# Kernel optimization log

Measured on AMD Instinct MI355X. Metric: run time of the kernel, lower is better.

The kernel has to match this reference:

```python
import math
import jax, jax.numpy as jnp
import numpy as np

B, T, C, H = 2, 1024, 1024, 16
D = C // H
BASE_SCALE = 0.03125
ATTN_ALPHA_INIT, MLP_ALPHA_INIT = 0.05, 0.05


def sinusoidal_embeddings(n, d):
    pos = jnp.arange(n, dtype=jnp.float32)[:, None]
    div = jnp.exp(jnp.arange(0, d, 2, dtype=jnp.float32) * (-math.log(10000.0) / d))
    emb = jnp.zeros((n, d), dtype=jnp.float32)
    emb = emb.at[:, 0::2].set(jnp.sin(pos * div))
    emb = emb.at[:, 1::2].set(jnp.cos(pos * div))
    return emb


def apply_rope(pos, q):
    # pos: (T, D); q: (B, H, T, D). Faithful to source: returns only the rotated-scaled component.
    pos = pos[-q.shape[2]:]
    d = q.shape[-1]
    sin, cos = pos[:, : d // 2], pos[:, d // 2 :]
    q_rot = jnp.stack((-q[..., 1::2], q[..., ::2]), axis=-1)  # (B,H,T,D/2,2)
    sc = jnp.stack((cos, sin), axis=-1)  # (T, D/2, 2)
    return (q_rot * sc).reshape(q.shape)


def justnorm(x):
    return x / jnp.linalg.norm(x, axis=-1, keepdims=True)


def setup_inputs() -> dict:
    key = jax.random.key(0)
    ks = jax.random.split(key, 14)
    w = lambda k, shape: jax.random.normal(k, shape, jnp.float32) * 0.02
    return {
        "h": jax.random.normal(ks[0], (B, T, C), jnp.float32),
        "Wq": w(ks[1], (C, C)),
        "Wk": w(ks[2], (C, C)),
        "Wv": w(ks[3], (C, C)),
        "Wo": w(ks[4], (C, C)),
        "Wfc": w(ks[5], (8 * C, C)),
        "Wproj": w(ks[6], (C, 4 * C)),
        "sqk": BASE_SCALE * jnp.ones(C) + w(ks[7], (C,)) * 0.05,
        "suv": jnp.ones(8 * C) + w(ks[8], (8 * C,)) * 0.05,
        "attn_alpha": BASE_SCALE * jnp.ones(C) + w(ks[9], (C,)) * 0.05,
        "mlp_alpha": BASE_SCALE * jnp.ones(C) + w(ks[10], (C,)) * 0.05,
        "thr_c": 1.6 * jnp.ones(H) + w(ks[11], (H,)) * 0.5,
        "stp": 10.0 * jnp.ones(H),
    }


def reference(h, Wq, Wk, Wv, Wo, Wfc, Wproj, sqk, suv, attn_alpha, mlp_alpha, thr_c, stp):
    softmax_scale = math.sqrt(D)  # nGPT uses sqrt(head_dim) since q,k are unit-normalized

    # --- attention branch (no pre-norm in nGPT mode) ---
    q = (h @ Wq.T).reshape(B, T, H, D).transpose(0, 2, 1, 3)  # (B,H,T,D)
    k = (h @ Wk.T).reshape(B, T, H, D).transpose(0, 2, 1, 3)
    v = (h @ Wv.T).reshape(B, T, H, D).transpose(0, 2, 1, 3)

    pos = sinusoidal_embeddings(T, D)
    q = apply_rope(pos, q)
    k = apply_rope(pos, k)

    sqk_s = (sqk * (1.0 / BASE_SCALE)).reshape(1, H, 1, D)
    q = sqk_s * justnorm(q)
    k = sqk_s * justnorm(k)

    scores = jnp.einsum("bhqd,bhkd->bhqk", q, k) * softmax_scale  # (B,H,T,T)
    causal = jnp.tril(jnp.ones((T, T), dtype=bool))
    w = jax.nn.softmax(jnp.where(causal, scores, -1e9), axis=-1)
    # soft score threshold: per-head sigmoid gate on raw scores, then renormalize
    gate = jax.nn.sigmoid(stp[None, :, None, None] * (scores - thr_c[None, :, None, None]))
    w = w * gate
    w = w / jnp.sum(w, axis=-1, keepdims=True)

    y = jnp.einsum("bhqk,bhkd->bhqd", w, v).transpose(0, 2, 1, 3).reshape(B, T, C)
    h_att = y @ Wo.T

    lr = jnp.abs(attn_alpha * (ATTN_ALPHA_INIT / BASE_SCALE))
    A = justnorm(h)
    Bn = justnorm(h_att)
    h = justnorm(A + lr * (Bn - A))

    # --- MLP branch ---
    uv = h @ Wfc.T  # (B,T,8C)
    uv = (suv * math.sqrt(C)) * uv
    u, vv = jnp.split(uv, 2, axis=-1)
    x_mlp = u * (vv * jax.nn.sigmoid(vv))
    h_mlp = x_mlp @ Wproj.T

    lr2 = jnp.abs(mlp_alpha * (MLP_ALPHA_INIT / BASE_SCALE))
    A = justnorm(h)
    Bn = justnorm(h_mlp)
    h = justnorm(A + lr2 * (Bn - A))
    return h
```

## Files before the change

kernel.cpp:

```cpp
#include <hip/hip_runtime.h>
#include <hip/hip_bf16.h>
#include <math.h>

typedef _Float16 f16x8 __attribute__((ext_vector_type(8)));
typedef float f32x4 __attribute__((ext_vector_type(4)));
typedef float f32x2 __attribute__((ext_vector_type(2)));
typedef unsigned short u16;
typedef unsigned int u32;
typedef u16 u16x4 __attribute__((ext_vector_type(4)));
typedef u16 u16x8 __attribute__((ext_vector_type(8)));

#define DEVI static __device__ __forceinline__
#define LDSS 72
#define MB (1u << 20)

DEVI u16 f2h(float f) {
    _Float16 h = (_Float16)f;
    return __builtin_bit_cast(u16, h);
}
DEVI float h2f(u16 u) {
    return (float)__builtin_bit_cast(_Float16, u);
}
DEVI f32x4 mfma16(f16x8 a, f16x8 b, f32x4 c) {
    return __builtin_amdgcn_mfma_f32_16x16x32_f16(a, b, c, 0, 0, 0);
}
DEVI void gload16(const u16* g, u16* l) {
    __builtin_amdgcn_global_load_lds((const __attribute__((address_space(1))) void*)g,
                                     (__attribute__((address_space(3))) void*)l, 16, 0, 0);
}

DEVI void stage128(const u16* __restrict__ g, size_t row0, int ldg, int k0, u16* lds) {
    int t = threadIdx.x;
    const u16* src = g + (row0 + (size_t)(t >> 3)) * (size_t)ldg + k0 + (t & 7) * 8;
    u16* dst = lds + (t >> 6) * 512;
#pragma unroll
    for (int is = 0; is < 4; is++)
        gload16(src + (size_t)is * 32 * ldg, dst + is * 2048);
}

DEVI void gemm128_core(const u16* __restrict__ A, const u16* __restrict__ B,
                       int ldk, int kbeg, int kend, int m0, int n0,
                       u16* As, u16* Bs, f32x4 acc[4][4]) {
    int lane = threadIdx.x & 63, w = threadIdx.x >> 6;
    int wm = (w >> 1) * 64, wn = (w & 1) * 64;
    int lrow = lane & 15, lg = lane >> 4;
    for (int k0 = kbeg; k0 < kend; k0 += 64) {
        __syncthreads();
        stage128(A, m0, ldk, k0, As);
        stage128(B, n0, ldk, k0, Bs);
        __syncthreads();
#pragma unroll
        for (int ks = 0; ks < 2; ks++) {
            f16x8 af[4], bf[4];
#pragma unroll
            for (int i = 0; i < 4; i++) {
                af[i] = *reinterpret_cast<f16x8*>(&As[(wm + i * 16 + lrow) * 64 + ks * 32 + lg * 8]);
                bf[i] = *reinterpret_cast<f16x8*>(&Bs[(wn + i * 16 + lrow) * 64 + ks * 32 + lg * 8]);
            }
#pragma unroll
            for (int i = 0; i < 4; i++)
#pragma unroll
                for (int j = 0; j < 4; j++)
                    acc[i][j] = mfma16(af[i], bf[j], acc[i][j]);
        }
    }
}

__global__ void cvt_kernel(const float* __restrict__ h, const float* __restrict__ Wq,
                           const float* __restrict__ Wk, const float* __restrict__ Wv,
                           const float* __restrict__ Wo, const float* __restrict__ Wfc,
                           const float* __restrict__ Wproj, u16* __restrict__ dst) {
    int bid = blockIdx.x;
    const float* src;
    size_t doff;
    int sb;
    if (bid < 1024)      { src = h;     sb = 0;    doff = 0; }
    else if (bid < 1536) { src = Wq;    sb = 1024; doff = 2097152; }
    else if (bid < 2048) { src = Wk;    sb = 1536; doff = 3145728; }
    else if (bid < 2560) { src = Wv;    sb = 2048; doff = 4194304; }
    else if (bid < 3072) { src = Wo;    sb = 2560; doff = 5242880; }
    else if (bid < 7168) { src = Wfc;   sb = 3072; doff = 10485760; }
    else                 { src = Wproj; sb = 7168; doff = 6291456; }
    size_t idx = (size_t)(bid - sb) * 2048 + threadIdx.x * 8;
    f32x4 a = *reinterpret_cast<const f32x4*>(src + idx);
    f32x4 b = *reinterpret_cast<const f32x4*>(src + idx + 4);
    u16x8 o;
    o[0] = f2h(a[0]); o[1] = f2h(a[1]); o[2] = f2h(a[2]); o[3] = f2h(a[3]);
    o[4] = f2h(b[0]); o[5] = f2h(b[1]); o[6] = f2h(b[2]); o[7] = f2h(b[3]);
    *reinterpret_cast<u16x8*>(dst + doff + idx) = o;
}

__global__ __launch_bounds__(256, 2) void qkv_h_kernel(
    const u16* __restrict__ hb, const u16* __restrict__ Wqh, const u16* __restrict__ Wkh,
    const u16* __restrict__ Wvh, u16* __restrict__ qb, u16* __restrict__ kb, u16* __restrict__ vb) {
    __shared__ u16 As[128 * 64];
    __shared__ u16 Bs[128 * 64];
    int z = blockIdx.z;
    const u16* W = (z == 0) ? Wqh : (z == 1) ? Wkh : Wvh;
    u16* dst = (z == 0) ? qb : (z == 1) ? kb : vb;
    int m0 = blockIdx.y * 128, n0 = blockIdx.x * 128;
    f32x4 acc[4][4];
    f32x4 zf = {0.f, 0.f, 0.f, 0.f};
#pragma unroll
    for (int i = 0; i < 4; i++)
#pragma unroll
        for (int j = 0; j < 4; j++) acc[i][j] = zf;
    gemm128_core(hb, W, 1024, 0, 1024, m0, n0, As, Bs, acc);
    int lane = threadIdx.x & 63, w = threadIdx.x >> 6;
    int wm = (w >> 1) * 64, wn = (w & 1) * 64;
    int lrow = lane & 15, lg = lane >> 4;
#pragma unroll
    for (int i = 0; i < 4; i++)
#pragma unroll
        for (int j = 0; j < 4; j++)
#pragma unroll
            for (int r = 0; r < 4; r++) {
                int m = m0 + wm + i * 16 + lg * 4 + r;
                int n = n0 + wn + j * 16 + lrow;
                dst[(size_t)m * 1024 + n] = f2h(acc[i][j][r]);
            }
}

__global__ __launch_bounds__(256, 2) void gemm_h_kernel(
    const u16* __restrict__ A, const u16* __restrict__ B, u16* __restrict__ out,
    int ldk, int ksplit, int osplit, int N) {
    __shared__ u16 As[128 * 64];
    __shared__ u16 Bs[128 * 64];
    int z = blockIdx.z;
    int m0 = blockIdx.y * 128, n0 = blockIdx.x * 128;
    f32x4 acc[4][4];
    f32x4 zf = {0.f, 0.f, 0.f, 0.f};
#pragma unroll
    for (int i = 0; i < 4; i++)
#pragma unroll
        for (int j = 0; j < 4; j++) acc[i][j] = zf;
    gemm128_core(A, B, ldk, z * ksplit, (z + 1) * ksplit, m0, n0, As, Bs, acc);
    u16* o = out + (size_t)z * osplit;
    int lane = threadIdx.x & 63, w = threadIdx.x >> 6;
    int wm = (w >> 1) * 64, wn = (w & 1) * 64;
    int lrow = lane & 15, lg = lane >> 4;
#pragma unroll
    for (int i = 0; i < 4; i++)
#pragma unroll
        for (int j = 0; j < 4; j++)
#pragma unroll
            for (int r = 0; r < 4; r++) {
                int m = m0 + wm + i * 16 + lg * 4 + r;
                int n = n0 + wn + j * 16 + lrow;
                o[(size_t)m * N + n] = f2h(acc[i][j][r]);
            }
}

__global__ void qkprep_kernel(u16* __restrict__ qb, u16* __restrict__ kb,
                              const float* __restrict__ sqk) {
    u16* buf = blockIdx.z ? kb : qb;
    int pair = blockIdx.x * 4 + (threadIdx.x >> 6);
    int m = pair >> 4, hh = pair & 15;
    int tt = m & 1023;
    int d = threadIdx.x & 63;
    size_t off = (size_t)m * 1024 + hh * 64 + d;
    float x = h2f(buf[off]);
    float xn = __shfl_xor(x, 1);
    int j = (d & 1) ? ((d - 1) >> 1) : (32 + (d >> 1));
    float dv = exp2f(-(float)(j >> 1) * 0.41524101186092029f);
    float ang = (float)tt * dv;
    float e = (j & 1) ? cosf(ang) : sinf(ang);
    float xr = (d & 1) ? (xn * e) : (-xn * e);
    float ss = xr * xr;
#pragma unroll
    for (int o = 1; o < 64; o <<= 1) ss += __shfl_xor(ss, o);
    float sc = rsqrtf(ss) * sqk[hh * 64 + d] * 32.0f;
    buf[off] = f2h(xr * sc);
}

__global__ __launch_bounds__(128) void attn_kernel(
    const u16* __restrict__ qb, const u16* __restrict__ kb, const u16* __restrict__ vb,
    const float* __restrict__ thr_c, const float* __restrict__ stp,
    float* __restrict__ yp, f32x2* __restrict__ mden) {
    const int T = 1024, C = 1024;
    int qt = 31 - (blockIdx.x >> 1);
    int c = blockIdx.x & 1;
    int bh = blockIdx.y;
    int b = bh >> 4, hh = bh & 15;
    int q0 = qt * 32;
    int nkt = (q0 >> 6) + 1;
    __shared__ u16 Vt[64 * LDSS];
    __shared__ u16 Ps[32 * LDSS];
    int t = threadIdx.x;
    int lane = t & 63, w = t >> 6;
    int lrow = lane & 15, lg = lane >> 4, lk = lg * 8;

    const u16* qrowp = qb + (size_t)(b * T + q0 + w * 16 + lrow) * C + hh * 64;
    f16x8 qfr[2];
    qfr[0] = *reinterpret_cast<const f16x8*>(qrowp + lk);
    qfr[1] = *reinterpret_cast<const f16x8*>(qrowp + 32 + lk);

    float thr = thr_c[hh], st = stp[hh];
    float st8 = st * 8.0f, stthr = st * thr;
    float mrun = -1e30f, den = 0.f;
    f32x4 yacc[4];
    f32x4 zf = {0.f, 0.f, 0.f, 0.f};
#pragma unroll
    for (int i = 0; i < 4; i++) yacc[i] = zf;
    int qg = q0 + w * 16 + lrow;

    for (int kt = c; kt < nkt; kt += 2) {
        int kv0 = kt << 6;
        __syncthreads();
        {
            int kvp = t & 31, db = t >> 5;
            const u16* src = vb + (size_t)(b * T + kv0 + 2 * kvp) * C + hh * 64 + db * 16;
#pragma unroll
            for (int dd = 0; dd < 4; dd++) {
                u16x4 a = *reinterpret_cast<const u16x4*>(src + dd * 4);
                u16x4 bb = *reinterpret_cast<const u16x4*>(src + C + dd * 4);
#pragma unroll
                for (int e = 0; e < 4; e++) {
                    u32 v = (u32)a[e] | ((u32)bb[e] << 16);
                    *reinterpret_cast<u32*>(&Vt[(db * 16 + dd * 4 + e) * LDSS + 2 * kvp]) = v;
                }
            }
        }

        f32x4 sacc[4];
#pragma unroll
        for (int f = 0; f < 4; f++) sacc[f] = zf;
#pragma unroll
        for (int ks = 0; ks < 2; ks++)
#pragma unroll
            for (int f = 0; f < 4; f++) {
                f16x8 kfr = *reinterpret_cast<const f16x8*>(
                    kb + (size_t)(b * T + kv0 + f * 16 + lrow) * C + hh * 64 + ks * 32 + lk);
                sacc[f] = mfma16(kfr, qfr[ks], sacc[f]);
            }
        __syncthreads();

        float svv[16];
        float tmax = -1e30f;
        bool last = (kt == nkt - 1);
#pragma unroll
        for (int f = 0; f < 4; f++)
#pragma unroll
            for (int r = 0; r < 4; r++) {
                float sv = sacc[f][r];
                float s = sv * 8.0f;
                float z = stthr - st8 * sv;
                float l = __logf(1.0f + __expf(z));
                float sp = s - ((z > 15.f) ? z : l);
                if (last) {
                    int kvg = kv0 + f * 16 + lg * 4 + r;
                    if (kvg > qg) sp = -1e30f;
                }
                svv[f * 4 + r] = sp;
                tmax = fmaxf(tmax, sp);
            }
        tmax = fmaxf(tmax, __shfl_xor(tmax, 16));
        tmax = fmaxf(tmax, __shfl_xor(tmax, 32));
        float mnew = fmaxf(mrun, tmax);
        float alpha = __expf(mrun - mnew);
        float tden = 0.f;
        u16 pu[16];
#pragma unroll
        for (int i = 0; i < 16; i++) {
            float p = __expf(svv[i] - mnew);
            u16 ph = f2h(p);
            pu[i] = ph;
            tden += h2f(ph);
        }
        tden += __shfl_xor(tden, 16);
        tden += __shfl_xor(tden, 32);
        den = den * alpha + tden;
        mrun = mnew;

#pragma unroll
        for (int f = 0; f < 4; f++) {
            u16x4 u = {pu[f * 4 + 0], pu[f * 4 + 1], pu[f * 4 + 2], pu[f * 4 + 3]};
            *reinterpret_cast<u16x4*>(&Ps[(w * 16 + lrow) * LDSS + f * 16 + lg * 4]) = u;
        }
        float a4[4];
#pragma unroll
        for (int r = 0; r < 4; r++) a4[r] = __shfl(alpha, lg * 4 + r);
#pragma unroll
        for (int nf = 0; nf < 4; nf++)
#pragma unroll
            for (int r = 0; r < 4; r++) yacc[nf][r] *= a4[r];

#pragma unroll
        for (int ks = 0; ks < 2; ks++) {
            f16x8 pf = *reinterpret_cast<f16x8*>(&Ps[(w * 16 + lrow) * LDSS + ks * 32 + lk]);
#pragma unroll
            for (int nf = 0; nf < 4; nf++) {
                f16x8 vf = *reinterpret_cast<f16x8*>(&Vt[(nf * 16 + lrow) * LDSS + ks * 32 + lk]);
                yacc[nf] = mfma16(pf, vf, yacc[nf]);
            }
        }
    }
    float* ypc = yp + (size_t)c * 2097152;
#pragma unroll
    for (int nf = 0; nf < 4; nf++)
#pragma unroll
        for (int r = 0; r < 4; r++) {
            int qrow = q0 + w * 16 + lg * 4 + r;
            ypc[(size_t)(b * T + qrow) * C + hh * 64 + nf * 16 + lrow] = yacc[nf][r];
        }
    if (lg == 0) {
        f32x2 md;
        md[0] = mrun; md[1] = den;
        mden[((size_t)c * 32 + bh) * 1024 + (q0 + w * 16 + lrow)] = md;
    }
}

__global__ void attn_merge_kernel(const float* __restrict__ yp, const f32x2* __restrict__ mden,
                                  u16* __restrict__ y) {
    int row = blockIdx.x;
    int b = row >> 10, tr = row & 1023;
    int t = threadIdx.x;
#pragma unroll
    for (int i = 0; i < 4; i++) {
        int idx = t + 256 * i;
        int hh = idx >> 6;
        f32x2 md0 = mden[((size_t)0 * 32 + b * 16 + hh) * 1024 + tr];
        f32x2 md1 = mden[((size_t)1 * 32 + b * 16 + hh) * 1024 + tr];
        float M = fmaxf(md0[0], md1[0]);
        float w0 = __expf(md0[0] - M), w1 = __expf(md1[0] - M);
        float dn = md0[1] * w0 + md1[1] * w1;
        size_t off = (size_t)row * 1024 + idx;
        float v = (yp[off] * w0 + yp[off + 2097152] * w1) / dn;
        y[off] = f2h(v);
    }
}

__global__ __launch_bounds__(256, 2) void fc_silu_kernel(
    const u16* __restrict__ h1h, const u16* __restrict__ Wfch,
    const float* __restrict__ suv, u16* __restrict__ xmlp) {
    __shared__ u16 As[128 * 64];
    __shared__ u16 Bu[128 * 64];
    __shared__ u16 Bv[128 * 64];
    int m0 = blockIdx.y * 128, n0 = blockIdx.x * 128;
    f32x4 au[4][4], av[4][4];
    f32x4 zf = {0.f, 0.f, 0.f, 0.f};
#pragma unroll
    for (int i = 0; i < 4; i++)
#pragma unroll
        for (int j = 0; j < 4; j++) { au[i][j] = zf; av[i][j] = zf; }
    int lane = threadIdx.x & 63, w = threadIdx.x >> 6;
    int wm = (w >> 1) * 64, wn = (w & 1) * 64;
    int lrow = lane & 15, lg = lane >> 4;
    for (int k0 = 0; k0 < 1024; k0 += 64) {
        __syncthreads();
        stage128(h1h, m0, 1024, k0, As);
        stage128(Wfch, n0, 1024, k0, Bu);
        stage128(Wfch, 4096 + n0, 1024, k0, Bv);
        __syncthreads();
#pragma unroll
        for (int ks = 0; ks < 2; ks++) {
            f16x8 af[4], bu[4], bv[4];
#pragma unroll
            for (int i = 0; i < 4; i++) {
                af[i] = *reinterpret_cast<f16x8*>(&As[(wm + i * 16 + lrow) * 64 + ks * 32 + lg * 8]);
                bu[i] = *reinterpret_cast<f16x8*>(&Bu[(wn + i * 16 + lrow) * 64 + ks * 32 + lg * 8]);
                bv[i] = *reinterpret_cast<f16x8*>(&Bv[(wn + i * 16 + lrow) * 64 + ks * 32 + lg * 8]);
            }
#pragma unroll
            for (int i = 0; i < 4; i++)
#pragma unroll
                for (int j = 0; j < 4; j++) {
                    au[i][j] = mfma16(af[i], bu[j], au[i][j]);
                    av[i][j] = mfma16(af[i], bv[j], av[i][j]);
                }
        }
    }
#pragma unroll
    for (int i = 0; i < 4; i++)
#pragma unroll
        for (int j = 0; j < 4; j++) {
            int n = n0 + wn + j * 16 + lrow;
            float su = suv[n] * 32.0f;
            float sv = suv[4096 + n] * 32.0f;
#pragma unroll
            for (int r = 0; r < 4; r++) {
                int m = m0 + wm + i * 16 + lg * 4 + r;
                float uu = au[i][j][r] * su;
                float vv = av[i][j][r] * sv;
                float sig = 1.0f / (1.0f + __expf(-vv));
                xmlp[(size_t)m * 4096 + n] = f2h(uu * vv * sig);
            }
        }
}

__global__ void normres_kernel(const float* __restrict__ base, const u16* __restrict__ dparts,
                               int nparts, int pstride, const float* __restrict__ alpha,
                               float* __restrict__ outf, u16* __restrict__ outh) {
    int row = blockIdx.x;
    int t = threadIdx.x;
    const float* pb = base + (size_t)row * 1024;
    float xb[4], xd[4];
    float ssb = 0.f, ssd = 0.f;
#pragma unroll
    for (int i = 0; i < 4; i++) {
        size_t off = (size_t)row * 1024 + t + 256 * i;
        xb[i] = pb[t + 256 * i];
        float d = 0.f;
        for (int p = 0; p < nparts; p++) d += h2f(dparts[off + (size_t)p * pstride]);
        xd[i] = d;
        ssb += xb[i] * xb[i];
        ssd += xd[i] * xd[i];
    }
#pragma unroll
    for (int o = 1; o < 64; o <<= 1) { ssb += __shfl_xor(ssb, o); ssd += __shfl_xor(ssd, o); }
    __shared__ float red[8];
    int w = t >> 6;
    if ((t & 63) == 0) { red[w * 2] = ssb; red[w * 2 + 1] = ssd; }
    __syncthreads();
    ssb = red[0] + red[2] + red[4] + red[6];
    ssd = red[1] + red[3] + red[5] + red[7];
    float rb = rsqrtf(ssb), rd = rsqrtf(ssd);
    float c[4];
    float ssc = 0.f;
#pragma unroll
    for (int i = 0; i < 4; i++) {
        float a = xb[i] * rb;
        float bb = xd[i] * rd;
        float lr = fabsf(alpha[t + 256 * i] * 1.6f);
        float cv = a + lr * (bb - a);
        c[i] = cv;
        ssc += cv * cv;
    }
#pragma unroll
    for (int o = 1; o < 64; o <<= 1) ssc += __shfl_xor(ssc, o);
    __syncthreads();
    if ((t & 63) == 0) red[w] = ssc;
    __syncthreads();
    ssc = red[0] + red[1] + red[2] + red[3];
    float rc = rsqrtf(ssc);
#pragma unroll
    for (int i = 0; i < 4; i++) {
        float v = c[i] * rc;
        size_t off = (size_t)row * 1024 + t + 256 * i;
        outf[off] = v;
        if (outh) outh[off] = f2h(v);
    }
}

extern "C" void kernel_launch(void* const* d_in, const int* in_sizes, int n_in,
                              void* d_out, int out_size, void* d_ws, size_t ws_size,
                              hipStream_t stream) {
    const float* h = (const float*)d_in[0];
    const float* Wq = (const float*)d_in[1];
    const float* Wk = (const float*)d_in[2];
    const float* Wv = (const float*)d_in[3];
    const float* Wo = (const float*)d_in[4];
    const float* Wfc = (const float*)d_in[5];
    const float* Wproj = (const float*)d_in[6];
    const float* sqk = (const float*)d_in[7];
    const float* suv = (const float*)d_in[8];
    const float* attn_alpha = (const float*)d_in[9];
    const float* mlp_alpha = (const float*)d_in[10];
    const float* thr_c = (const float*)d_in[11];
    const float* stp = (const float*)d_in[12];

    char* ws = (char*)d_ws;
    u16* f16heap = (u16*)ws;
    u16* hb     = f16heap + 0;
    u16* Wqh    = f16heap + 2097152;
    u16* Wkh    = f16heap + 3145728;
    u16* Wvh    = f16heap + 4194304;
    u16* Woh    = f16heap + 5242880;
    u16* Wprojh = f16heap + 6291456;
    u16* Wfch   = f16heap + 10485760;
    u16* partsP = Wfch;
    u16* qb   = (u16*)(ws + (size_t)36 * MB);
    u16* kb   = (u16*)(ws + (size_t)40 * MB);
    u16* vb   = (u16*)(ws + (size_t)44 * MB);
    u16* y    = (u16*)(ws + (size_t)48 * MB);
    float* yp = (float*)(ws + (size_t)52 * MB);
    u16* hattP = qb;
    float* h1 = (float*)(ws + (size_t)56 * MB);
    u16* h1h  = (u16*)(ws + (size_t)64 * MB);
    f32x2* mden = (f32x2*)(ws + (size_t)68 * MB);
    u16* xmlp = (u16*)(ws + (size_t)36 * MB);
    float* out = (float*)d_out;

    cvt_kernel<<<9216, 256, 0, stream>>>(h, Wq, Wk, Wv, Wo, Wfc, Wproj, f16heap);
    qkv_h_kernel<<<dim3(8, 16, 3), 256, 0, stream>>>(hb, Wqh, Wkh, Wvh, qb, kb, vb);
    qkprep_kernel<<<dim3(8192, 1, 2), 256, 0, stream>>>(qb, kb, sqk);
    attn_kernel<<<dim3(64, 32), 128, 0, stream>>>(qb, kb, vb, thr_c, stp, yp, mden);
    attn_merge_kernel<<<2048, 256, 0, stream>>>(yp, mden, y);
    gemm_h_kernel<<<dim3(8, 16, 2), 256, 0, stream>>>(y, Woh, hattP, 1024, 512, 2097152, 1024);
    normres_kernel<<<2048, 256, 0, stream>>>(h, hattP, 2, 2097152, attn_alpha, h1, h1h);
    fc_silu_kernel<<<dim3(32, 16), 256, 0, stream>>>(h1h, Wfch, suv, xmlp);
    gemm_h_kernel<<<dim3(8, 16, 4), 256, 0, stream>>>(xmlp, Wprojh, partsP, 4096, 1024, 2097152, 1024);
    normres_kernel<<<2048, 256, 0, stream>>>(h1, partsP, 4, 2097152, mlp_alpha, out, (u16*)nullptr);
}
```

Measured before the change: 210.0 us.

## Prefetch K/V into registers, double-buffer V, simplify gate math, split Wo GEMM

New measurement: 205.9 us. Within noise of the previous version (-1.9%).

```diff
diff --git a/kernel.cpp b/kernel.cpp
--- a/kernel.cpp
+++ b/kernel.cpp
@@ -184,11 +184,12 @@
     int b = bh >> 4, hh = bh & 15;
     int q0 = qt * 32;
     int nkt = (q0 >> 6) + 1;
-    __shared__ u16 Vt[64 * LDSS];
+    __shared__ u16 Vt[2][64 * LDSS];
     __shared__ u16 Ps[32 * LDSS];
     int t = threadIdx.x;
     int lane = t & 63, w = t >> 6;
     int lrow = lane & 15, lg = lane >> 4, lk = lg * 8;
+    int kvp = t & 31, db = t >> 5;
 
     const u16* qrowp = qb + (size_t)(b * T + q0 + w * 16 + lrow) * C + hh * 64;
     f16x8 qfr[2];
@@ -196,7 +197,7 @@
     qfr[1] = *reinterpret_cast<const f16x8*>(qrowp + 32 + lk);
 
     float thr = thr_c[hh], st = stp[hh];
-    float st8 = st * 8.0f, stthr = st * thr;
+    float stthr = st * thr;
     float mrun = -1e30f, den = 0.f;
     f32x4 yacc[4];
     f32x4 zf = {0.f, 0.f, 0.f, 0.f};
@@ -204,36 +205,59 @@
     for (int i = 0; i < 4; i++) yacc[i] = zf;
     int qg = q0 + w * 16 + lrow;
 
+    f16x8 kpre[8];
+    u16x4 vr[8];
+    const u16* kbase0 = kb + (size_t)(b * T + lrow) * C + hh * 64 + lk;
+    const u16* vbase0 = vb + (size_t)(b * T + 2 * kvp) * C + hh * 64 + db * 16;
+
+    if (c < nkt) {
+        const u16* kbase = kbase0 + (size_t)(c << 6) * C;
+        const u16* vsrc = vbase0 + (size_t)(c << 6) * C;
+#pragma unroll
+        for (int ks = 0; ks < 2; ks++)
+#pragma unroll
+            for (int f = 0; f < 4; f++)
+                kpre[ks * 4 + f] = *reinterpret_cast<const f16x8*>(kbase + (size_t)(f * 16) * C + ks * 32);
+#pragma unroll
+        for (int dd = 0; dd < 4; dd++) {
+            vr[dd * 2] = *reinterpret_cast<const u16x4*>(vsrc + dd * 4);
+            vr[dd * 2 + 1] = *reinterpret_cast<const u16x4*>(vsrc + C + dd * 4);
+        }
+    }
+
     for (int kt = c; kt < nkt; kt += 2) {
         int kv0 = kt << 6;
-        __syncthreads();
-        {
-            int kvp = t & 31, db = t >> 5;
-            const u16* src = vb + (size_t)(b * T + kv0 + 2 * kvp) * C + hh * 64 + db * 16;
+        u16* VB = Vt[(kt >> 1) & 1];
+#pragma unroll
+        for (int dd = 0; dd < 4; dd++)
+#pragma unroll
+            for (int e = 0; e < 4; e++) {
+                u32 v = (u32)vr[dd * 2][e] | ((u32)vr[dd * 2 + 1][e] << 16);
+                *reinterpret_cast<u32*>(&VB[(db * 16 + dd * 4 + e) * LDSS + 2 * kvp]) = v;
+            }
+        f32x4 sacc[4];
+#pragma unroll
+        for (int f = 0; f < 4; f++) sacc[f] = zf;
+#pragma unroll
+        for (int ks = 0; ks < 2; ks++)
+#pragma unroll
+            for (int f = 0; f < 4; f++)
+                sacc[f] = mfma16(kpre[ks * 4 + f], qfr[ks], sacc[f]);
+
+        if (kt + 2 < nkt) {
+            const u16* kbase = kbase0 + (size_t)((kt + 2) << 6) * C;
+            const u16* vsrc = vbase0 + (size_t)((kt + 2) << 6) * C;
+#pragma unroll
+            for (int ks = 0; ks < 2; ks++)
+#pragma unroll
+                for (int f = 0; f < 4; f++)
+                    kpre[ks * 4 + f] = *reinterpret_cast<const f16x8*>(kbase + (size_t)(f * 16) * C + ks * 32);
 #pragma unroll
             for (int dd = 0; dd < 4; dd++) {
-                u16x4 a = *reinterpret_cast<const u16x4*>(src + dd * 4);
-                u16x4 bb = *reinterpret_cast<const u16x4*>(src + C + dd * 4);
-#pragma unroll
-                for (int e = 0; e < 4; e++) {
-                    u32 v = (u32)a[e] | ((u32)bb[e] << 16);
-                    *reinterpret_cast<u32*>(&Vt[(db * 16 + dd * 4 + e) * LDSS + 2 * kvp]) = v;
-                }
-            }
-        }
-
-        f32x4 sacc[4];
-#pragma unroll
-        for (int f = 0; f < 4; f++) sacc[f] = zf;
-#pragma unroll
-        for (int ks = 0; ks < 2; ks++)
-#pragma unroll
-            for (int f = 0; f < 4; f++) {
-                f16x8 kfr = *reinterpret_cast<const f16x8*>(
-                    kb + (size_t)(b * T + kv0 + f * 16 + lrow) * C + hh * 64 + ks * 32 + lk);
-                sacc[f] = mfma16(kfr, qfr[ks], sacc[f]);
-            }
-        __syncthreads();
+                vr[dd * 2] = *reinterpret_cast<const u16x4*>(vsrc + dd * 4);
+                vr[dd * 2 + 1] = *reinterpret_cast<const u16x4*>(vsrc + C + dd * 4);
+            }
+        }
 
         float svv[16];
         float tmax = -1e30f;
@@ -242,27 +266,28 @@
         for (int f = 0; f < 4; f++)
 #pragma unroll
             for (int r = 0; r < 4; r++) {
-                float sv = sacc[f][r];
-                float s = sv * 8.0f;
-                float z = stthr - st8 * sv;
-                float l = __logf(1.0f + __expf(z));
-                float sp = s - ((z > 15.f) ? z : l);
+                float s = sacc[f][r] * 8.0f;
                 if (last) {
                     int kvg = kv0 + f * 16 + lg * 4 + r;
-                    if (kvg > qg) sp = -1e30f;
+                    if (kvg > qg) s = -1e30f;
                 }
-                svv[f * 4 + r] = sp;
-                tmax = fmaxf(tmax, sp);
+                svv[f * 4 + r] = s;
+                tmax = fmaxf(tmax, s);
             }
         tmax = fmaxf(tmax, __shfl_xor(tmax, 16));
         tmax = fmaxf(tmax, __shfl_xor(tmax, 32));
-        float mnew = fmaxf(mrun, tmax);
+        float zM = stthr - st * tmax;
+        float spM = tmax - __logf(1.0f + __expf(zM));
+        float mnew = fmaxf(mrun, spM);
         float alpha = __expf(mrun - mnew);
         float tden = 0.f;
         u16 pu[16];
 #pragma unroll
         for (int i = 0; i < 16; i++) {
-            float p = __expf(svv[i] - mnew);
+            float s = svv[i];
+            float e2 = __expf(s - mnew);
+            float eg = __expf(stthr - st * s);
+            float p = e2 * __builtin_amdgcn_rcpf(1.0f + eg);
             u16 ph = f2h(p);
             pu[i] = ph;
             tden += h2f(ph);
@@ -285,12 +310,14 @@
 #pragma unroll
             for (int r = 0; r < 4; r++) yacc[nf][r] *= a4[r];
 
+        __syncthreads();
+
 #pragma unroll
         for (int ks = 0; ks < 2; ks++) {
             f16x8 pf = *reinterpret_cast<f16x8*>(&Ps[(w * 16 + lrow) * LDSS + ks * 32 + lk]);
 #pragma unroll
             for (int nf = 0; nf < 4; nf++) {
-                f16x8 vf = *reinterpret_cast<f16x8*>(&Vt[(nf * 16 + lrow) * LDSS + ks * 32 + lk]);
+                f16x8 vf = *reinterpret_cast<f16x8*>(&VB[(nf * 16 + lrow) * LDSS + ks * 32 + lk]);
                 yacc[nf] = mfma16(pf, vf, yacc[nf]);
             }
         }
@@ -474,11 +501,11 @@
     u16* vb   = (u16*)(ws + (size_t)44 * MB);
     u16* y    = (u16*)(ws + (size_t)48 * MB);
     float* yp = (float*)(ws + (size_t)52 * MB);
-    u16* hattP = qb;
-    float* h1 = (float*)(ws + (size_t)56 * MB);
-    u16* h1h  = (u16*)(ws + (size_t)64 * MB);
     f32x2* mden = (f32x2*)(ws + (size_t)68 * MB);
-    u16* xmlp = (u16*)(ws + (size_t)36 * MB);
+    u16* hattP = (u16*)(ws + (size_t)52 * MB);
+    float* h1 = (float*)(ws + (size_t)36 * MB);
+    u16* h1h  = (u16*)(ws + (size_t)44 * MB);
+    u16* xmlp = (u16*)(ws + (size_t)52 * MB);
     float* out = (float*)d_out;
 
     cvt_kernel<<<9216, 256, 0, stream>>>(h, Wq, Wk, Wv, Wo, Wfc, Wproj, f16heap);
@@ -486,8 +513,8 @@
     qkprep_kernel<<<dim3(8192, 1, 2), 256, 0, stream>>>(qb, kb, sqk);
     attn_kernel<<<dim3(64, 32), 128, 0, stream>>>(qb, kb, vb, thr_c, stp, yp, mden);
     attn_merge_kernel<<<2048, 256, 0, stream>>>(yp, mden, y);
-    gemm_h_kernel<<<dim3(8, 16, 2), 256, 0, stream>>>(y, Woh, hattP, 1024, 512, 2097152, 1024);
-    normres_kernel<<<2048, 256, 0, stream>>>(h, hattP, 2, 2097152, attn_alpha, h1, h1h);
+    gemm_h_kernel<<<dim3(8, 16, 4), 256, 0, stream>>>(y, Woh, hattP, 1024, 256, 2097152, 1024);
+    normres_kernel<<<2048, 256, 0, stream>>>(h, hattP, 4, 2097152, attn_alpha, h1, h1h);
     fc_silu_kernel<<<dim3(32, 16), 256, 0, stream>>>(h1h, Wfch, suv, xmlp);
     gemm_h_kernel<<<dim3(8, 16, 4), 256, 0, stream>>>(xmlp, Wprojh, partsP, 4096, 1024, 2097152, 1024);
     normres_kernel<<<2048, 256, 0, stream>>>(h1, partsP, 4, 2097152, mlp_alpha, out, (u16*)nullptr);
```
